# Kernel optimization log

Hardware: AMD Instinct MI355X
Metric: run time of the kernel (lower is better)

Reference implementation:

```python
import jax, jax.numpy as jnp
import numpy as np

N_HEADS = 16


def setup_inputs() -> dict:
    key = jax.random.key(0)
    ks = jax.random.split(key, 10)
    B, M, N, C, D = 2, 2048, 2048, 1024, 1024
    s = 0.02
    return {
        "kv": jax.random.normal(ks[0], (B, M, C), jnp.float32),
        "q": jax.random.normal(ks[1], (B, N, D), jnp.float32),
        "Wk": jax.random.normal(ks[2], (C, D), jnp.float32) * s,
        "bk": jnp.zeros((D,), jnp.float32),
        "Wq": jax.random.normal(ks[3], (D, D), jnp.float32) * s,
        "bq": jnp.zeros((D,), jnp.float32),
        "Wv": jax.random.normal(ks[4], (C, D), jnp.float32) * s,
        "bv": jnp.zeros((D,), jnp.float32),
        "Wp": jax.random.normal(ks[5], (D, D), jnp.float32) * s,
        "bp": jnp.zeros((D,), jnp.float32),
    }


def reference(kv, q, Wk, bk, Wq, bq, Wv, bv, Wp, bp):
    B, M, C = kv.shape
    B2, N, D = q.shape
    H = N_HEADS
    hd = D // H
    # projections (weights stored as [in, out]; torch Linear is x @ W.T + b with W [out,in])
    k = (kv @ Wk + bk).reshape(B, M, H, hd).transpose(0, 2, 1, 3)  # [B,H,M,hd]
    qh = (q @ Wq + bq).reshape(B, N, H, hd).transpose(0, 2, 1, 3)  # [B,H,N,hd]
    v = (kv @ Wv + bv).reshape(B, M, H, hd).transpose(0, 2, 1, 3)  # [B,H,M,hd]
    scale = 1.0 / jnp.sqrt(jnp.asarray(hd, k.dtype))
    att = jnp.einsum("bhnd,bhmd->bhnm", qh, k) * scale
    att = jax.nn.softmax(att, axis=-1)
    y = jnp.einsum("bhnm,bhmd->bhnd", att, v)  # [B,H,N,hd]
    y = y.transpose(0, 2, 1, 3).reshape(B, N, D)
    return y @ Wp + bp
```

## Files before the change

### kernel.cpp

```cpp
#include <hip/hip_runtime.h>

#define DV 1024
#define HD 64

typedef short v4s __attribute__((ext_vector_type(4)));
typedef short v8s __attribute__((ext_vector_type(8)));
typedef float v4f __attribute__((ext_vector_type(4)));
typedef int   v2i __attribute__((ext_vector_type(2)));

__device__ __forceinline__ short f2bf(float x){
  unsigned u = __float_as_uint(x);
  u += 0x7FFFu + ((u >> 16) & 1u);
  return (short)(u >> 16);
}

__device__ __forceinline__ int swz(int lane){
  return (((lane & 7) ^ (lane >> 3)) << 3);
}

__global__ __launch_bounds__(256) void cvt2(const float* __restrict__ xa,
                                            const float* __restrict__ xb,
                                            short* __restrict__ ya,
                                            short* __restrict__ yb, int n){
  const float* x = blockIdx.y ? xb : xa;
  short* y = blockIdx.y ? yb : ya;
  int stride = gridDim.x * 256 * 4;
  for (int i = (blockIdx.x * 256 + threadIdx.x) * 4; i < n; i += stride){
    float4 v = *(const float4*)(x + i);
    v4s s; s.x = f2bf(v.x); s.y = f2bf(v.y); s.z = f2bf(v.z); s.w = f2bf(v.w);
    *(v4s*)(y + i) = s;
  }
}

__global__ __launch_bounds__(256) void tcvt4(
    const float* __restrict__ W0, const float* __restrict__ W1,
    const float* __restrict__ W2, const float* __restrict__ W3,
    short* __restrict__ T0, short* __restrict__ T1,
    short* __restrict__ T2, short* __restrict__ T3){
  const float* W; short* Wt;
  switch (blockIdx.z){
    case 0: W = W0; Wt = T0; break;
    case 1: W = W1; Wt = T1; break;
    case 2: W = W2; Wt = T2; break;
    default: W = W3; Wt = T3; break;
  }
  __shared__ short L[64 * 68];
  const int t = threadIdx.x;
  const int k0 = blockIdx.y * 64, n0 = blockIdx.x * 64;
  const int rr = t >> 4, cc = (t & 15) * 4;
  #pragma unroll
  for (int j = 0; j < 4; j++){
    int r = rr + j * 16;
    float4 v = *(const float4*)(W + (size_t)(k0 + r) * DV + n0 + cc);
    v4s s; s.x = f2bf(v.x); s.y = f2bf(v.y); s.z = f2bf(v.z); s.w = f2bf(v.w);
    *(v4s*)&L[r * 68 + cc] = s;
  }
  __syncthreads();
  #pragma unroll
  for (int j = 0; j < 4; j++){
    int n = rr + j * 16;
    v4s s;
    s.x = L[(cc + 0) * 68 + n];
    s.y = L[(cc + 1) * 68 + n];
    s.z = L[(cc + 2) * 68 + n];
    s.w = L[(cc + 3) * 68 + n];
    *(v4s*)(Wt + (size_t)(n0 + n) * DV + k0 + cc) = s;
  }
}

template<typename OUT_T>
__device__ __forceinline__ void gemm_tile(
    const short* __restrict__ A, const short* __restrict__ Bt,
    const float* __restrict__ bias, OUT_T* __restrict__ C,
    int M, int N, int K, float out_scale, int m0, int n0, bool bias_row)
{
  __shared__ short As[128 * 64];
  __shared__ short Bs[128 * 64];
  const int tid = threadIdx.x;
  const int wave = tid >> 6, lane = tid & 63;
  const int quad = lane >> 4, l15 = lane & 15;
  const int wr = (wave >> 1) * 64, wc = (wave & 1) * 64;
  const int srow = lane >> 3;
  const int sw = swz(lane);
  const v4f vzero = {0.f, 0.f, 0.f, 0.f};

  const short* pa[4]; const short* pb[4];
  #pragma unroll
  for (int ii = 0; ii < 4; ii++){
    int i = wave * 4 + ii;
    pa[ii] = A  + (size_t)(m0 + i * 8 + srow) * K + sw;
    pb[ii] = Bt + (size_t)(n0 + i * 8 + srow) * K + sw;
  }

  v8s ra[4], rb[4];
  #pragma unroll
  for (int ii = 0; ii < 4; ii++){
    ra[ii] = *(const v8s*)(pa[ii]);
    rb[ii] = *(const v8s*)(pb[ii]);
  }

  v4f acc[4][4];
  #pragma unroll
  for (int i = 0; i < 4; i++)
    #pragma unroll
    for (int j = 0; j < 4; j++)
      acc[i][j] = vzero;

  for (int kt = 0; kt < K; kt += 64){
    __syncthreads();
    #pragma unroll
    for (int ii = 0; ii < 4; ii++){
      int i = wave * 4 + ii;
      *(v8s*)&As[i * 512 + lane * 8] = ra[ii];
      *(v8s*)&Bs[i * 512 + lane * 8] = rb[ii];
    }
    __syncthreads();
    if (kt + 64 < K){
      #pragma unroll
      for (int ii = 0; ii < 4; ii++){
        ra[ii] = *(const v8s*)(pa[ii] + kt + 64);
        rb[ii] = *(const v8s*)(pb[ii] + kt + 64);
      }
    }
    #pragma unroll
    for (int ks = 0; ks < 2; ks++){
      v8s a[4], b[4];
      #pragma unroll
      for (int mt = 0; mt < 4; mt++)
        a[mt] = *(const v8s*)&As[(wr + mt * 16 + l15) * 64 + (((ks * 4 + quad) ^ (l15 & 7)) << 3)];
      #pragma unroll
      for (int nt = 0; nt < 4; nt++)
        b[nt] = *(const v8s*)&Bs[(wc + nt * 16 + l15) * 64 + (((ks * 4 + quad) ^ (l15 & 7)) << 3)];
      #pragma unroll
      for (int mt = 0; mt < 4; mt++)
        #pragma unroll
        for (int nt = 0; nt < 4; nt++)
          acc[mt][nt] = __builtin_amdgcn_mfma_f32_16x16x32_bf16(a[mt], b[nt], acc[mt][nt], 0, 0, 0);
    }
  }

  #pragma unroll
  for (int mt = 0; mt < 4; mt++){
    #pragma unroll
    for (int nt = 0; nt < 4; nt++){
      int row = m0 + wr + mt * 16 + quad * 4;
      int col = n0 + wc + nt * 16 + l15;
      float bcol = bias_row ? 0.0f : bias[col];
      #pragma unroll
      for (int r = 0; r < 4; r++){
        float bv = bias_row ? bias[row + r] : bcol;
        float v = (acc[mt][nt][r] + bv) * out_scale;
        if (sizeof(OUT_T) == 2)
          ((short*)C)[(size_t)(row + r) * N + col] = f2bf(v);
        else
          ((float*)C)[(size_t)(row + r) * N + col] = v;
      }
    }
  }
}

__global__ __launch_bounds__(256, 3) void proj3(
    const short* __restrict__ qb, const short* __restrict__ kvb,
    const short* __restrict__ Wqt, const short* __restrict__ Wkt,
    const short* __restrict__ Wvt,
    const float* __restrict__ bq, const float* __restrict__ bk,
    const float* __restrict__ bv,
    short* __restrict__ Qp, short* __restrict__ Kp, short* __restrict__ VT,
    float qscale)
{
  int bid = blockIdx.x;
  const short *A, *Bt; const float* bias; short* C;
  int M, N, m0, n0; float scale; bool brow;
  if (bid < 512){
    int z = bid >> 8, l = bid & 255;
    M = 4096; N = 1024; m0 = (l & 31) * 128; n0 = (l >> 5) * 128;
    A = z ? kvb : qb; Bt = z ? Wkt : Wqt; bias = z ? bk : bq;
    C = z ? Kp : Qp; scale = z ? 1.0f : qscale; brow = false;
  } else {
    int l = bid - 512;
    M = 1024; N = 4096; m0 = (l >> 5) * 128; n0 = (l & 31) * 128;
    A = Wvt; Bt = kvb; bias = bv; C = VT; scale = 1.0f; brow = true;
  }
  gemm_tile<short>(A, Bt, bias, C, M, N, 1024, scale, m0, n0, brow);
}

__global__ __launch_bounds__(256, 2) void gemm_f32(
    const short* __restrict__ A, const short* __restrict__ Bt,
    const float* __restrict__ bias, float* __restrict__ C)
{
  __shared__ short As[128 * 64];
  __shared__ short Bs[64 * 64];
  const int tid = threadIdx.x;
  const int wave = tid >> 6, lane = tid & 63;
  const int quad = lane >> 4, l15 = lane & 15;
  const int bid = blockIdx.x;
  const int m0 = (bid & 31) * 128, n0 = (bid >> 5) * 64;
  const int wr = (wave >> 1) * 64, wc = (wave & 1) * 32;
  const int srow = lane >> 3;
  const int sw = swz(lane);
  const int K = 1024;
  const v4f vzero = {0.f, 0.f, 0.f, 0.f};

  const short* pa[4]; const short* pb[2];
  #pragma unroll
  for (int ii = 0; ii < 4; ii++)
    pa[ii] = A + (size_t)(m0 + (wave * 4 + ii) * 8 + srow) * K + sw;
  #pragma unroll
  for (int ii = 0; ii < 2; ii++)
    pb[ii] = Bt + (size_t)(n0 + (wave * 2 + ii) * 8 + srow) * K + sw;

  v8s ra[4], rb[2];
  #pragma unroll
  for (int ii = 0; ii < 4; ii++) ra[ii] = *(const v8s*)(pa[ii]);
  #pragma unroll
  for (int ii = 0; ii < 2; ii++) rb[ii] = *(const v8s*)(pb[ii]);

  v4f acc[4][2];
  #pragma unroll
  for (int i = 0; i < 4; i++){ acc[i][0] = vzero; acc[i][1] = vzero; }

  for (int kt = 0; kt < K; kt += 64){
    __syncthreads();
    #pragma unroll
    for (int ii = 0; ii < 4; ii++)
      *(v8s*)&As[(wave * 4 + ii) * 512 + lane * 8] = ra[ii];
    #pragma unroll
    for (int ii = 0; ii < 2; ii++)
      *(v8s*)&Bs[(wave * 2 + ii) * 512 + lane * 8] = rb[ii];
    __syncthreads();
    if (kt + 64 < K){
      #pragma unroll
      for (int ii = 0; ii < 4; ii++) ra[ii] = *(const v8s*)(pa[ii] + kt + 64);
      #pragma unroll
      for (int ii = 0; ii < 2; ii++) rb[ii] = *(const v8s*)(pb[ii] + kt + 64);
    }
    #pragma unroll
    for (int ks = 0; ks < 2; ks++){
      v8s a[4], b[2];
      #pragma unroll
      for (int mt = 0; mt < 4; mt++)
        a[mt] = *(const v8s*)&As[(wr + mt * 16 + l15) * 64 + (((ks * 4 + quad) ^ (l15 & 7)) << 3)];
      #pragma unroll
      for (int nt = 0; nt < 2; nt++)
        b[nt] = *(const v8s*)&Bs[(wc + nt * 16 + l15) * 64 + (((ks * 4 + quad) ^ (l15 & 7)) << 3)];
      #pragma unroll
      for (int mt = 0; mt < 4; mt++)
        #pragma unroll
        for (int nt = 0; nt < 2; nt++)
          acc[mt][nt] = __builtin_amdgcn_mfma_f32_16x16x32_bf16(a[mt], b[nt], acc[mt][nt], 0, 0, 0);
    }
  }

  #pragma unroll
  for (int mt = 0; mt < 4; mt++){
    #pragma unroll
    for (int nt = 0; nt < 2; nt++){
      int row = m0 + wr + mt * 16 + quad * 4;
      int col = n0 + wc + nt * 16 + l15;
      float bcol = bias[col];
      #pragma unroll
      for (int r = 0; r < 4; r++)
        C[(size_t)(row + r) * 1024 + col] = acc[mt][nt][r] + bcol;
    }
  }
}

__global__ __launch_bounds__(256, 3) void attn(
    const short* __restrict__ Qp, const short* __restrict__ Kp,
    const short* __restrict__ Vt, short* __restrict__ Y)
{
  __shared__ short Ks[64 * 64];
  __shared__ short Vs[64 * 68];
  const int tid = threadIdx.x;
  const int wave = tid >> 6, lane = tid & 63;
  const int quad = lane >> 4, l15 = lane & 15;
  const int gid = blockIdx.x;
  const int qi = gid >> 5, bh = gid & 31;
  const int h = bh & 15, b = bh >> 4;
  const int n0 = qi * 128;
  const int srow = lane >> 3;
  const int c8 = (lane & 7) * 8;
  const int sw = swz(lane);
  const size_t rowbase = (size_t)b * 2048;
  const v4f vzero = {0.f, 0.f, 0.f, 0.f};

  v8s qf[2][2];
  #pragma unroll
  for (int qt = 0; qt < 2; qt++){
    const short* qrow = Qp + (rowbase + n0 + wave * 32 + qt * 16 + l15) * DV + h * HD + quad * 8;
    qf[qt][0] = *(const v8s*)(qrow);
    qf[qt][1] = *(const v8s*)(qrow + 32);
  }

  const short* pk[2]; const short* pv[2];
  #pragma unroll
  for (int ii = 0; ii < 2; ii++){
    int i = wave * 2 + ii;
    pk[ii] = Kp + (rowbase + i * 8 + srow) * DV + h * HD + sw;
    pv[ii] = Vt + (size_t)(h * HD + i * 8 + srow) * 4096 + rowbase + c8;
  }
  v8s rk[2], rv[2];
  #pragma unroll
  for (int ii = 0; ii < 2; ii++){ rk[ii] = *(const v8s*)(pk[ii]); rv[ii] = *(const v8s*)(pv[ii]); }

  v4f o[4][2];
  #pragma unroll
  for (int dt = 0; dt < 4; dt++){ o[dt][0] = vzero; o[dt][1] = vzero; }
  float lsum[2] = {0.0f, 0.0f};

  for (int kt = 0; kt < 32; kt++){
    __syncthreads();
    #pragma unroll
    for (int ii = 0; ii < 2; ii++){
      int i = wave * 2 + ii;
      *(v8s*)&Ks[i * 512 + lane * 8] = rk[ii];
      *(v8s*)&Vs[(i * 8 + srow) * 68 + c8] = rv[ii];
    }
    __syncthreads();
    if (kt < 31){
      #pragma unroll
      for (int ii = 0; ii < 2; ii++){
        rk[ii] = *(const v8s*)(pk[ii] + (size_t)(kt + 1) * 64 * DV);
        rv[ii] = *(const v8s*)(pv[ii] + (kt + 1) * 64);
      }
    }

    v4f s[2][4];
    #pragma unroll
    for (int qt = 0; qt < 2; qt++)
      #pragma unroll
      for (int kvt = 0; kvt < 4; kvt++) s[qt][kvt] = vzero;
    #pragma unroll
    for (int ks = 0; ks < 2; ks++){
      v8s a[4];
      #pragma unroll
      for (int kvt = 0; kvt < 4; kvt++)
        a[kvt] = *(const v8s*)&Ks[(kvt * 16 + l15) * 64 + (((ks * 4 + quad) ^ (l15 & 7)) << 3)];
      #pragma unroll
      for (int kvt = 0; kvt < 4; kvt++)
        #pragma unroll
        for (int qt = 0; qt < 2; qt++)
          s[qt][kvt] = __builtin_amdgcn_mfma_f32_16x16x32_bf16(a[kvt], qf[qt][ks], s[qt][kvt], 0, 0, 0);
    }

    v4s pf[2][4];
    #pragma unroll
    for (int qt = 0; qt < 2; qt++)
      #pragma unroll
      for (int kvt = 0; kvt < 4; kvt++){
        float p0 = __builtin_amdgcn_exp2f(s[qt][kvt][0]);
        float p1 = __builtin_amdgcn_exp2f(s[qt][kvt][1]);
        float p2 = __builtin_amdgcn_exp2f(s[qt][kvt][2]);
        float p3 = __builtin_amdgcn_exp2f(s[qt][kvt][3]);
        lsum[qt] += (p0 + p1) + (p2 + p3);
        unsigned u0 = __float_as_uint(p0) + 0x8000u;
        unsigned u1 = __float_as_uint(p1) + 0x8000u;
        unsigned u2 = __float_as_uint(p2) + 0x8000u;
        unsigned u3 = __float_as_uint(p3) + 0x8000u;
        v2i pi;
        pi.x = (int)__builtin_amdgcn_perm(u1, u0, 0x07060302u);
        pi.y = (int)__builtin_amdgcn_perm(u3, u2, 0x07060302u);
        pf[qt][kvt] = __builtin_bit_cast(v4s, pi);
      }

    #pragma unroll
    for (int ks = 0; ks < 4; ks++){
      v4s a[4];
      #pragma unroll
      for (int dt = 0; dt < 4; dt++)
        a[dt] = *(const v4s*)&Vs[(dt * 16 + l15) * 68 + ks * 16 + quad * 4];
      #pragma unroll
      for (int dt = 0; dt < 4; dt++)
        #pragma unroll
        for (int qt = 0; qt < 2; qt++)
          o[dt][qt] = __builtin_amdgcn_mfma_f32_16x16x16bf16_1k(a[dt], pf[qt][ks], o[dt][qt], 0, 0, 0);
    }
  }

  #pragma unroll
  for (int qt = 0; qt < 2; qt++){
    float ls = lsum[qt];
    ls += __shfl_xor(ls, 16);
    ls += __shfl_xor(ls, 32);
    float inv = 1.0f / ls;
    size_t row = rowbase + n0 + wave * 32 + qt * 16 + l15;
    #pragma unroll
    for (int dt = 0; dt < 4; dt++){
      int col = h * HD + dt * 16 + quad * 4;
      unsigned p0 = (unsigned short)f2bf(o[dt][qt][0] * inv) |
                    ((unsigned)(unsigned short)f2bf(o[dt][qt][1] * inv) << 16);
      unsigned p1 = (unsigned short)f2bf(o[dt][qt][2] * inv) |
                    ((unsigned)(unsigned short)f2bf(o[dt][qt][3] * inv) << 16);
      *(unsigned*)(Y + row * DV + col)     = p0;
      *(unsigned*)(Y + row * DV + col + 2) = p1;
    }
  }
}

extern "C" void kernel_launch(void* const* d_in, const int* in_sizes, int n_in,
                              void* d_out, int out_size, void* d_ws, size_t ws_size,
                              hipStream_t stream) {
  const float* kv = (const float*)d_in[0];
  const float* q  = (const float*)d_in[1];
  const float* Wk = (const float*)d_in[2];
  const float* bk = (const float*)d_in[3];
  const float* Wq = (const float*)d_in[4];
  const float* bq = (const float*)d_in[5];
  const float* Wv = (const float*)d_in[6];
  const float* bv = (const float*)d_in[7];
  const float* Wp = (const float*)d_in[8];
  const float* bp = (const float*)d_in[9];

  const size_t E  = 4194304;
  const size_t WE = 1048576;
  short* p   = (short*)d_ws;
  short* kvb = p; p += E;
  short* qb  = p; p += E;
  short* Wkt = p; p += WE;
  short* Wqt = p; p += WE;
  short* Wvt = p; p += WE;
  short* Wpt = p; p += WE;
  short* Kp  = p; p += E;
  short* Qp  = p; p += E;
  short* VT  = p; p += E;
  short* Yb  = p; p += E;

  cvt2<<<dim3(512, 2), 256, 0, stream>>>(kv, q, kvb, qb, (int)E);
  tcvt4<<<dim3(16, 16, 4), 256, 0, stream>>>(Wk, Wq, Wv, Wp, Wkt, Wqt, Wvt, Wpt);

  proj3<<<768, 256, 0, stream>>>(qb, kvb, Wqt, Wkt, Wvt, bq, bk, bv,
                                 Qp, Kp, VT, 0.18033688011f);

  attn<<<512, 256, 0, stream>>>(Qp, Kp, VT, Yb);

  gemm_f32<<<512, 256, 0, stream>>>(Yb, Wpt, bp, (float*)d_out);
}
```

Measured before the change: 206.2 us.

## Double-buffer attention K/V tiles, add MFMA priority hints, fuse prep kernels

The attention loop now keeps two LDS buffers for K and V. The next tile is written into the alternate buffer while the current one is consumed, so each iteration needs one barrier instead of two. s_setprio raises wave priority around the MFMA sections to improve interleaving between waves. The activation conversion and the weight transpose-convert kernels are merged into one launch, saving a kernel launch. LDS use in attention doubles, which may reduce occupancy at launch bounds of 3 blocks per CU.

```diff
diff --git a/kernel.cpp b/kernel.cpp
--- a/kernel.cpp
+++ b/kernel.cpp
@@ -18,33 +18,35 @@
   return (((lane & 7) ^ (lane >> 3)) << 3);
 }
 
-__global__ __launch_bounds__(256) void cvt2(const float* __restrict__ xa,
-                                            const float* __restrict__ xb,
-                                            short* __restrict__ ya,
-                                            short* __restrict__ yb, int n){
-  const float* x = blockIdx.y ? xb : xa;
-  short* y = blockIdx.y ? yb : ya;
-  int stride = gridDim.x * 256 * 4;
-  for (int i = (blockIdx.x * 256 + threadIdx.x) * 4; i < n; i += stride){
-    float4 v = *(const float4*)(x + i);
-    v4s s; s.x = f2bf(v.x); s.y = f2bf(v.y); s.z = f2bf(v.z); s.w = f2bf(v.w);
-    *(v4s*)(y + i) = s;
-  }
-}
-
-__global__ __launch_bounds__(256) void tcvt4(
+__global__ __launch_bounds__(256) void prep(
+    const float* __restrict__ kv, const float* __restrict__ q,
+    short* __restrict__ kvb, short* __restrict__ qb,
     const float* __restrict__ W0, const float* __restrict__ W1,
     const float* __restrict__ W2, const float* __restrict__ W3,
     short* __restrict__ T0, short* __restrict__ T1,
-    short* __restrict__ T2, short* __restrict__ T3){
+    short* __restrict__ T2, short* __restrict__ T3, int n)
+{
+  __shared__ short L[64 * 68];
+  const int z = blockIdx.z;
+  if (z >= 4){
+    const float* x = (z == 5) ? q : kv;
+    short* y = (z == 5) ? qb : kvb;
+    int bid = blockIdx.y * 16 + blockIdx.x;
+    int stride = 256 * 256 * 4;
+    for (int i = (bid * 256 + threadIdx.x) * 4; i < n; i += stride){
+      float4 v = *(const float4*)(x + i);
+      v4s s; s.x = f2bf(v.x); s.y = f2bf(v.y); s.z = f2bf(v.z); s.w = f2bf(v.w);
+      *(v4s*)(y + i) = s;
+    }
+    return;
+  }
   const float* W; short* Wt;
-  switch (blockIdx.z){
+  switch (z){
     case 0: W = W0; Wt = T0; break;
     case 1: W = W1; Wt = T1; break;
     case 2: W = W2; Wt = T2; break;
     default: W = W3; Wt = T3; break;
   }
-  __shared__ short L[64 * 68];
   const int t = threadIdx.x;
   const int k0 = blockIdx.y * 64, n0 = blockIdx.x * 64;
   const int rr = t >> 4, cc = (t & 15) * 4;
@@ -58,13 +60,13 @@
   __syncthreads();
   #pragma unroll
   for (int j = 0; j < 4; j++){
-    int n = rr + j * 16;
+    int nn = rr + j * 16;
     v4s s;
-    s.x = L[(cc + 0) * 68 + n];
-    s.y = L[(cc + 1) * 68 + n];
-    s.z = L[(cc + 2) * 68 + n];
-    s.w = L[(cc + 3) * 68 + n];
-    *(v4s*)(Wt + (size_t)(n0 + n) * DV + k0 + cc) = s;
+    s.x = L[(cc + 0) * 68 + nn];
+    s.y = L[(cc + 1) * 68 + nn];
+    s.z = L[(cc + 2) * 68 + nn];
+    s.w = L[(cc + 3) * 68 + nn];
+    *(v4s*)(Wt + (size_t)(n0 + nn) * DV + k0 + cc) = s;
   }
 }
 
@@ -269,8 +271,8 @@
     const short* __restrict__ Qp, const short* __restrict__ Kp,
     const short* __restrict__ Vt, short* __restrict__ Y)
 {
-  __shared__ short Ks[64 * 64];
-  __shared__ short Vs[64 * 68];
+  __shared__ short Ks[2][64 * 64];
+  __shared__ short Vs[2][64 * 68];
   const int tid = threadIdx.x;
   const int wave = tid >> 6, lane = tid & 63;
   const int quad = lane >> 4, l15 = lane & 15;
@@ -303,26 +305,44 @@
   #pragma unroll
   for (int ii = 0; ii < 2; ii++){ rk[ii] = *(const v8s*)(pk[ii]); rv[ii] = *(const v8s*)(pv[ii]); }
 
+  #pragma unroll
+  for (int ii = 0; ii < 2; ii++){
+    int i = wave * 2 + ii;
+    *(v8s*)&Ks[0][i * 512 + lane * 8] = rk[ii];
+    *(v8s*)&Vs[0][(i * 8 + srow) * 68 + c8] = rv[ii];
+  }
+  #pragma unroll
+  for (int ii = 0; ii < 2; ii++){
+    rk[ii] = *(const v8s*)(pk[ii] + (size_t)64 * DV);
+    rv[ii] = *(const v8s*)(pv[ii] + 64);
+  }
+  __syncthreads();
+
   v4f o[4][2];
   #pragma unroll
   for (int dt = 0; dt < 4; dt++){ o[dt][0] = vzero; o[dt][1] = vzero; }
   float lsum[2] = {0.0f, 0.0f};
 
+  int cur = 0;
   for (int kt = 0; kt < 32; kt++){
-    __syncthreads();
-    #pragma unroll
-    for (int ii = 0; ii < 2; ii++){
-      int i = wave * 2 + ii;
-      *(v8s*)&Ks[i * 512 + lane * 8] = rk[ii];
-      *(v8s*)&Vs[(i * 8 + srow) * 68 + c8] = rv[ii];
-    }
-    __syncthreads();
+    const short* Kr = Ks[cur];
+    const short* Vr = Vs[cur];
     if (kt < 31){
+      short* Kw = Ks[cur ^ 1];
+      short* Vw = Vs[cur ^ 1];
       #pragma unroll
       for (int ii = 0; ii < 2; ii++){
-        rk[ii] = *(const v8s*)(pk[ii] + (size_t)(kt + 1) * 64 * DV);
-        rv[ii] = *(const v8s*)(pv[ii] + (kt + 1) * 64);
+        int i = wave * 2 + ii;
+        *(v8s*)&Kw[i * 512 + lane * 8] = rk[ii];
+        *(v8s*)&Vw[(i * 8 + srow) * 68 + c8] = rv[ii];
       }
+      if (kt < 30){
+        #pragma unroll
+        for (int ii = 0; ii < 2; ii++){
+          rk[ii] = *(const v8s*)(pk[ii] + (size_t)(kt + 2) * 64 * DV);
+          rv[ii] = *(const v8s*)(pv[ii] + (kt + 2) * 64);
+        }
+      }
     }
 
     v4f s[2][4];
@@ -330,18 +350,20 @@
     for (int qt = 0; qt < 2; qt++)
       #pragma unroll
       for (int kvt = 0; kvt < 4; kvt++) s[qt][kvt] = vzero;
+    __builtin_amdgcn_s_setprio(1);
     #pragma unroll
     for (int ks = 0; ks < 2; ks++){
       v8s a[4];
       #pragma unroll
       for (int kvt = 0; kvt < 4; kvt++)
-        a[kvt] = *(const v8s*)&Ks[(kvt * 16 + l15) * 64 + (((ks * 4 + quad) ^ (l15 & 7)) << 3)];
+        a[kvt] = *(const v8s*)&Kr[(kvt * 16 + l15) * 64 + (((ks * 4 + quad) ^ (l15 & 7)) << 3)];
       #pragma unroll
       for (int kvt = 0; kvt < 4; kvt++)
         #pragma unroll
         for (int qt = 0; qt < 2; qt++)
           s[qt][kvt] = __builtin_amdgcn_mfma_f32_16x16x32_bf16(a[kvt], qf[qt][ks], s[qt][kvt], 0, 0, 0);
     }
+    __builtin_amdgcn_s_setprio(0);
 
     v4s pf[2][4];
     #pragma unroll
@@ -363,18 +385,23 @@
         pf[qt][kvt] = __builtin_bit_cast(v4s, pi);
       }
 
+    __builtin_amdgcn_s_setprio(1);
     #pragma unroll
     for (int ks = 0; ks < 4; ks++){
       v4s a[4];
       #pragma unroll
       for (int dt = 0; dt < 4; dt++)
-        a[dt] = *(const v4s*)&Vs[(dt * 16 + l15) * 68 + ks * 16 + quad * 4];
+        a[dt] = *(const v4s*)&Vr[(dt * 16 + l15) * 68 + ks * 16 + quad * 4];
       #pragma unroll
       for (int dt = 0; dt < 4; dt++)
         #pragma unroll
         for (int qt = 0; qt < 2; qt++)
           o[dt][qt] = __builtin_amdgcn_mfma_f32_16x16x16bf16_1k(a[dt], pf[qt][ks], o[dt][qt], 0, 0, 0);
     }
+    __builtin_amdgcn_s_setprio(0);
+
+    __syncthreads();
+    cur ^= 1;
   }
 
   #pragma unroll
@@ -425,8 +452,9 @@
   short* VT  = p; p += E;
   short* Yb  = p; p += E;
 
-  cvt2<<<dim3(512, 2), 256, 0, stream>>>(kv, q, kvb, qb, (int)E);
-  tcvt4<<<dim3(16, 16, 4), 256, 0, stream>>>(Wk, Wq, Wv, Wp, Wkt, Wqt, Wvt, Wpt);
+  prep<<<dim3(16, 16, 6), 256, 0, stream>>>(kv, q, kvb, qb,
+                                            Wk, Wq, Wv, Wp,
+                                            Wkt, Wqt, Wvt, Wpt, (int)E);
 
   proj3<<<768, 256, 0, stream>>>(qb, kvb, Wqt, Wkt, Wvt, bq, bk, bv,
                                  Qp, Kp, VT, 0.18033688011f);
```

New measurement: 217.7 us. 1.06x slower.

## Rewrite projection GEMM with 256x256 tiles and async global-to-LDS double buffering

Applied to the files above, without the earlier changes.

Replaces the 128x128 register-staged projection GEMM with a 512-thread, 256x256-tile kernel that loads global data straight into double-buffered LDS via global_load_lds. Loads for the next k-tile are interleaved with MFMA phases under explicit barriers, waitcnts and setprio. The aim is more reuse per tile and better overlap of memory with compute. In exchange it uses 128KB of dynamic LDS and launches only 192 blocks, which may underfill the GPU's compute units.

```diff
diff --git a/kernel.cpp b/kernel.cpp
--- a/kernel.cpp
+++ b/kernel.cpp
@@ -16,6 +16,13 @@
 
 __device__ __forceinline__ int swz(int lane){
   return (((lane & 7) ^ (lane >> 3)) << 3);
+}
+
+__device__ __forceinline__ void gload16(const short* g, short* l){
+  __builtin_amdgcn_global_load_lds(
+      (const __attribute__((address_space(1))) void*)g,
+      (__attribute__((address_space(3))) void*)l,
+      16, 0, 0);
 }
 
 __global__ __launch_bounds__(256) void cvt2(const float* __restrict__ xa,
@@ -68,98 +75,7 @@
   }
 }
 
-template<typename OUT_T>
-__device__ __forceinline__ void gemm_tile(
-    const short* __restrict__ A, const short* __restrict__ Bt,
-    const float* __restrict__ bias, OUT_T* __restrict__ C,
-    int M, int N, int K, float out_scale, int m0, int n0, bool bias_row)
-{
-  __shared__ short As[128 * 64];
-  __shared__ short Bs[128 * 64];
-  const int tid = threadIdx.x;
-  const int wave = tid >> 6, lane = tid & 63;
-  const int quad = lane >> 4, l15 = lane & 15;
-  const int wr = (wave >> 1) * 64, wc = (wave & 1) * 64;
-  const int srow = lane >> 3;
-  const int sw = swz(lane);
-  const v4f vzero = {0.f, 0.f, 0.f, 0.f};
-
-  const short* pa[4]; const short* pb[4];
-  #pragma unroll
-  for (int ii = 0; ii < 4; ii++){
-    int i = wave * 4 + ii;
-    pa[ii] = A  + (size_t)(m0 + i * 8 + srow) * K + sw;
-    pb[ii] = Bt + (size_t)(n0 + i * 8 + srow) * K + sw;
-  }
-
-  v8s ra[4], rb[4];
-  #pragma unroll
-  for (int ii = 0; ii < 4; ii++){
-    ra[ii] = *(const v8s*)(pa[ii]);
-    rb[ii] = *(const v8s*)(pb[ii]);
-  }
-
-  v4f acc[4][4];
-  #pragma unroll
-  for (int i = 0; i < 4; i++)
-    #pragma unroll
-    for (int j = 0; j < 4; j++)
-      acc[i][j] = vzero;
-
-  for (int kt = 0; kt < K; kt += 64){
-    __syncthreads();
-    #pragma unroll
-    for (int ii = 0; ii < 4; ii++){
-      int i = wave * 4 + ii;
-      *(v8s*)&As[i * 512 + lane * 8] = ra[ii];
-      *(v8s*)&Bs[i * 512 + lane * 8] = rb[ii];
-    }
-    __syncthreads();
-    if (kt + 64 < K){
-      #pragma unroll
-      for (int ii = 0; ii < 4; ii++){
-        ra[ii] = *(const v8s*)(pa[ii] + kt + 64);
-        rb[ii] = *(const v8s*)(pb[ii] + kt + 64);
-      }
-    }
-    #pragma unroll
-    for (int ks = 0; ks < 2; ks++){
-      v8s a[4], b[4];
-      #pragma unroll
-      for (int mt = 0; mt < 4; mt++)
-        a[mt] = *(const v8s*)&As[(wr + mt * 16 + l15) * 64 + (((ks * 4 + quad) ^ (l15 & 7)) << 3)];
-      #pragma unroll
-      for (int nt = 0; nt < 4; nt++)
-        b[nt] = *(const v8s*)&Bs[(wc + nt * 16 + l15) * 64 + (((ks * 4 + quad) ^ (l15 & 7)) << 3)];
-      #pragma unroll
-      for (int mt = 0; mt < 4; mt++)
-        #pragma unroll
-        for (int nt = 0; nt < 4; nt++)
-          acc[mt][nt] = __builtin_amdgcn_mfma_f32_16x16x32_bf16(a[mt], b[nt], acc[mt][nt], 0, 0, 0);
-    }
-  }
-
-  #pragma unroll
-  for (int mt = 0; mt < 4; mt++){
-    #pragma unroll
-    for (int nt = 0; nt < 4; nt++){
-      int row = m0 + wr + mt * 16 + quad * 4;
-      int col = n0 + wc + nt * 16 + l15;
-      float bcol = bias_row ? 0.0f : bias[col];
-      #pragma unroll
-      for (int r = 0; r < 4; r++){
-        float bv = bias_row ? bias[row + r] : bcol;
-        float v = (acc[mt][nt][r] + bv) * out_scale;
-        if (sizeof(OUT_T) == 2)
-          ((short*)C)[(size_t)(row + r) * N + col] = f2bf(v);
-        else
-          ((float*)C)[(size_t)(row + r) * N + col] = v;
-      }
-    }
-  }
-}
-
-__global__ __launch_bounds__(256, 3) void proj3(
+__global__ __launch_bounds__(512, 2) void proj8(
     const short* __restrict__ qb, const short* __restrict__ kvb,
     const short* __restrict__ Wqt, const short* __restrict__ Wkt,
     const short* __restrict__ Wvt,
@@ -168,20 +84,174 @@
     short* __restrict__ Qp, short* __restrict__ Kp, short* __restrict__ VT,
     float qscale)
 {
+  extern __shared__ short smem[];
+  short* const LA = smem;
+  short* const LB = smem + 32768;
+  const int tid = threadIdx.x;
+  const int wv = tid >> 6, lane = tid & 63;
+  const int quad = lane >> 4, l15 = lane & 15;
+  const int l7 = l15 & 7;
+  const int wm = wv >> 2, wn = wv & 3;
+  const int sw = swz(lane);
+  const int r8 = lane >> 3;
+  const int K = 1024, NT = 16;
+
   int bid = blockIdx.x;
   const short *A, *Bt; const float* bias; short* C;
   int M, N, m0, n0; float scale; bool brow;
-  if (bid < 512){
-    int z = bid >> 8, l = bid & 255;
-    M = 4096; N = 1024; m0 = (l & 31) * 128; n0 = (l >> 5) * 128;
+  if (bid < 128){
+    int z = bid >> 6, l = bid & 63;
+    M = 4096; N = 1024; m0 = (l & 15) * 256; n0 = (l >> 4) * 256;
     A = z ? kvb : qb; Bt = z ? Wkt : Wqt; bias = z ? bk : bq;
     C = z ? Kp : Qp; scale = z ? 1.0f : qscale; brow = false;
   } else {
-    int l = bid - 512;
-    M = 1024; N = 4096; m0 = (l >> 5) * 128; n0 = (l & 31) * 128;
+    int l = bid - 128;
+    M = 1024; N = 4096; m0 = (l & 3) * 256; n0 = (l >> 2) * 256;
     A = Wvt; Bt = kvb; bias = bv; C = VT; scale = 1.0f; brow = true;
   }
-  gemm_tile<short>(A, Bt, bias, C, M, N, 1024, scale, m0, n0, brow);
+  (void)M;
+
+  const short* pA = A  + (size_t)(m0 + wv * 8 + r8) * K + sw;
+  const short* pB = Bt + (size_t)(n0 + wv * 8 + r8) * K + sw;
+  const int ldsw = wv * 512;
+
+  v4f acc[2][4][4];
+  #pragma unroll
+  for (int mh = 0; mh < 2; mh++)
+    #pragma unroll
+    for (int mf = 0; mf < 4; mf++)
+      #pragma unroll
+      for (int nf = 0; nf < 4; nf++)
+        acc[mh][mf][nf] = (v4f){0.f, 0.f, 0.f, 0.f};
+
+  #pragma unroll
+  for (int c = 0; c < 4; c++){
+    gload16(pA + (size_t)c * 64 * K,      LA + c * 4096 + ldsw);
+    gload16(pB + (size_t)c * 64 * K,      LB + c * 4096 + ldsw);
+  }
+  #pragma unroll
+  for (int c = 0; c < 4; c++){
+    gload16(pA + (size_t)c * 64 * K + 64, LA + 16384 + c * 4096 + ldsw);
+    gload16(pB + (size_t)c * 64 * K + 64, LB + 16384 + c * 4096 + ldsw);
+  }
+  asm volatile("s_waitcnt vmcnt(8)" ::: "memory");
+  __builtin_amdgcn_s_barrier();
+  __builtin_amdgcn_sched_barrier(0);
+
+  v8s av[4], bw[4];
+  for (int t = 0; t < NT; t++){
+    const int b = t & 1, nb = b ^ 1;
+    const short* la = LA + b * 16384;
+    const short* lb = LB + b * 16384;
+    const int kt1 = (t + 1) * 64;
+    const bool st = (t >= 1) && (t + 1 < NT);
+
+    #pragma unroll
+    for (int mf = 0; mf < 4; mf++)
+      av[mf] = *(const v8s*)&la[(wm * 128 + mf * 16 + l15) * 64 + ((quad ^ l7) << 3)];
+    #pragma unroll
+    for (int nf = 0; nf < 4; nf++)
+      bw[nf] = *(const v8s*)&lb[(wn * 64 + nf * 16 + l15) * 64 + ((quad ^ l7) << 3)];
+    if (st){
+      gload16(pA + (size_t)0 * 64 * K + kt1, LA + nb * 16384 + 0 * 4096 + ldsw);
+      gload16(pA + (size_t)2 * 64 * K + kt1, LA + nb * 16384 + 2 * 4096 + ldsw);
+    }
+    __builtin_amdgcn_s_barrier();
+    asm volatile("s_waitcnt lgkmcnt(0)" ::: "memory");
+    __builtin_amdgcn_sched_barrier(0);
+    __builtin_amdgcn_s_setprio(1);
+    #pragma unroll
+    for (int mf = 0; mf < 4; mf++)
+      #pragma unroll
+      for (int nf = 0; nf < 4; nf++)
+        acc[0][mf][nf] = __builtin_amdgcn_mfma_f32_16x16x32_bf16(av[mf], bw[nf], acc[0][mf][nf], 0, 0, 0);
+    __builtin_amdgcn_s_setprio(0);
+    asm volatile("s_waitcnt vmcnt(2)" ::: "memory");
+    __builtin_amdgcn_s_barrier();
+    __builtin_amdgcn_sched_barrier(0);
+
+    #pragma unroll
+    for (int mf = 0; mf < 4; mf++)
+      av[mf] = *(const v8s*)&la[(wm * 128 + 64 + mf * 16 + l15) * 64 + ((quad ^ l7) << 3)];
+    if (st){
+      gload16(pB + (size_t)0 * 64 * K + kt1, LB + nb * 16384 + 0 * 4096 + ldsw);
+      gload16(pB + (size_t)1 * 64 * K + kt1, LB + nb * 16384 + 1 * 4096 + ldsw);
+    }
+    __builtin_amdgcn_s_barrier();
+    asm volatile("s_waitcnt lgkmcnt(0)" ::: "memory");
+    __builtin_amdgcn_sched_barrier(0);
+    __builtin_amdgcn_s_setprio(1);
+    #pragma unroll
+    for (int mf = 0; mf < 4; mf++)
+      #pragma unroll
+      for (int nf = 0; nf < 4; nf++)
+        acc[1][mf][nf] = __builtin_amdgcn_mfma_f32_16x16x32_bf16(av[mf], bw[nf], acc[1][mf][nf], 0, 0, 0);
+    __builtin_amdgcn_s_setprio(0);
+    __builtin_amdgcn_s_barrier();
+    __builtin_amdgcn_sched_barrier(0);
+
+    #pragma unroll
+    for (int mf = 0; mf < 4; mf++)
+      av[mf] = *(const v8s*)&la[(wm * 128 + mf * 16 + l15) * 64 + (((4 + quad) ^ l7) << 3)];
+    #pragma unroll
+    for (int nf = 0; nf < 4; nf++)
+      bw[nf] = *(const v8s*)&lb[(wn * 64 + nf * 16 + l15) * 64 + (((4 + quad) ^ l7) << 3)];
+    if (st){
+      gload16(pB + (size_t)2 * 64 * K + kt1, LB + nb * 16384 + 2 * 4096 + ldsw);
+      gload16(pB + (size_t)3 * 64 * K + kt1, LB + nb * 16384 + 3 * 4096 + ldsw);
+    }
+    __builtin_amdgcn_s_barrier();
+    asm volatile("s_waitcnt lgkmcnt(0)" ::: "memory");
+    __builtin_amdgcn_sched_barrier(0);
+    __builtin_amdgcn_s_setprio(1);
+    #pragma unroll
+    for (int mf = 0; mf < 4; mf++)
+      #pragma unroll
+      for (int nf = 0; nf < 4; nf++)
+        acc[0][mf][nf] = __builtin_amdgcn_mfma_f32_16x16x32_bf16(av[mf], bw[nf], acc[0][mf][nf], 0, 0, 0);
+    __builtin_amdgcn_s_setprio(0);
+    __builtin_amdgcn_s_barrier();
+    __builtin_amdgcn_sched_barrier(0);
+
+    #pragma unroll
+    for (int mf = 0; mf < 4; mf++)
+      av[mf] = *(const v8s*)&la[(wm * 128 + 64 + mf * 16 + l15) * 64 + (((4 + quad) ^ l7) << 3)];
+    if (st){
+      gload16(pA + (size_t)1 * 64 * K + kt1, LA + nb * 16384 + 1 * 4096 + ldsw);
+      gload16(pA + (size_t)3 * 64 * K + kt1, LA + nb * 16384 + 3 * 4096 + ldsw);
+    }
+    __builtin_amdgcn_s_barrier();
+    asm volatile("s_waitcnt lgkmcnt(0)" ::: "memory");
+    __builtin_amdgcn_sched_barrier(0);
+    __builtin_amdgcn_s_setprio(1);
+    #pragma unroll
+    for (int mf = 0; mf < 4; mf++)
+      #pragma unroll
+      for (int nf = 0; nf < 4; nf++)
+        acc[1][mf][nf] = __builtin_amdgcn_mfma_f32_16x16x32_bf16(av[mf], bw[nf], acc[1][mf][nf], 0, 0, 0);
+    __builtin_amdgcn_s_setprio(0);
+    asm volatile("s_waitcnt vmcnt(2)" ::: "memory");
+    __builtin_amdgcn_s_barrier();
+    __builtin_amdgcn_sched_barrier(0);
+  }
+
+  #pragma unroll
+  for (int mh = 0; mh < 2; mh++){
+    #pragma unroll
+    for (int mf = 0; mf < 4; mf++){
+      #pragma unroll
+      for (int nf = 0; nf < 4; nf++){
+        int row = m0 + wm * 128 + mh * 64 + mf * 16 + quad * 4;
+        int col = n0 + wn * 64 + nf * 16 + l15;
+        float bcol = brow ? 0.0f : bias[col];
+        #pragma unroll
+        for (int r = 0; r < 4; r++){
+          float bvv = brow ? bias[row + r] : bcol;
+          C[(size_t)(row + r) * N + col] = f2bf((acc[mh][mf][nf][r] + bvv) * scale);
+        }
+      }
+    }
+  }
 }
 
 __global__ __launch_bounds__(256, 2) void gemm_f32(
@@ -425,11 +495,18 @@
   short* VT  = p; p += E;
   short* Yb  = p; p += E;
 
+  static int s_attr = 0;
+  if (!s_attr){
+    hipFuncSetAttribute((const void*)proj8,
+                        hipFuncAttributeMaxDynamicSharedMemorySize, 131072);
+    s_attr = 1;
+  }
+
   cvt2<<<dim3(512, 2), 256, 0, stream>>>(kv, q, kvb, qb, (int)E);
   tcvt4<<<dim3(16, 16, 4), 256, 0, stream>>>(Wk, Wq, Wv, Wp, Wkt, Wqt, Wvt, Wpt);
 
-  proj3<<<768, 256, 0, stream>>>(qb, kvb, Wqt, Wkt, Wvt, bq, bk, bv,
-                                 Qp, Kp, VT, 0.18033688011f);
+  proj8<<<192, 512, 131072, stream>>>(qb, kvb, Wqt, Wkt, Wvt, bq, bk, bv,
+                                      Qp, Kp, VT, 0.18033688011f);
 
   attn<<<512, 256, 0, stream>>>(Qp, Kp, VT, Yb);
 
```

After: 213.0 us. 3.3% more time.
